# Performance work log

Hardware: AMD Instinct MI355X
Metric: run time of the kernel (lower is better)

Reference implementation:

```python
import jax, jax.numpy as jnp
import numpy as np

U, B, D = 1024, 8, 512
H, HD = 8, 64
CL, RC = 64, 4            # chunk length, right-context per chunk
C = U // CL               # 16 chunks
R, S, M = C * RC, C, C - 1
Q, KV = R + U + S, M + R + U
PE = 2 * U - 1
NEG_INF = -1e8


def _chunk_mask():
    # True = disallowed connection. Query rows = [right_context(R), utterance(U), summary(S)];
    # key cols = [memory(M), right_context(R), utterance(U)].
    mask = np.ones((Q, KV), dtype=bool)
    for c in range(C):
        cols = []
        cols += list(range(0, c))                                  # memory of preceding chunks
        cols += list(range(M + c * RC, M + (c + 1) * RC))          # own right context
        u0 = max(0, c - 1) * CL                                    # one left-context chunk
        cols += list(range(M + R + u0, M + R + (c + 1) * CL))      # utterance up to own chunk
        cols = np.array(cols)
        rows = np.concatenate([
            np.arange(c * RC, (c + 1) * RC),                       # right-context queries
            np.arange(R + c * CL, R + (c + 1) * CL),               # utterance queries
            np.array([R + U + c]),                                 # summary query
        ])
        mask[np.ix_(rows, cols)] = False
    return jnp.asarray(mask)


def _xavier(key, shape):
    fan_in, fan_out = shape[-1], shape[0]
    a = (6.0 / (fan_in + fan_out)) ** 0.5
    return jax.random.uniform(key, shape, jnp.float32, -a, a)


def setup_inputs() -> dict:
    key = jax.random.key(0)
    ks = jax.random.split(key, 16)
    return {
        "utterance": jax.random.normal(ks[0], (U, B, D), jnp.float32),
        "lengths": jax.random.randint(ks[1], (B,), U // 2, U + 1),
        "right_context": jax.random.normal(ks[2], (R, B, D), jnp.float32),
        "summary": jax.random.normal(ks[3], (S, B, D), jnp.float32),
        "memory": jax.random.normal(ks[4], (M, B, D), jnp.float32),
        "attention_mask": _chunk_mask(),
        "pos_emb": jax.random.normal(ks[5], (PE, D), jnp.float32),
        "W_kv": _xavier(ks[6], (2 * D, D)),
        "b_kv": jnp.zeros((2 * D,), jnp.float32),
        "W_q": _xavier(ks[7], (D, D)),
        "b_q": jnp.zeros((D,), jnp.float32),
        "W_out": _xavier(ks[8], (D, D)),
        "b_out": jnp.zeros((D,), jnp.float32),
        "W_pos": _xavier(ks[9], (D, D)),
        "pos_bias_u": _xavier(ks[10], (H, HD)),
        "pos_bias_v": _xavier(ks[11], (H, HD)),
    }


def reference(utterance, lengths, right_context, summary, memory, attention_mask,
              pos_emb, W_kv, b_kv, W_q, b_q, W_out, b_out, W_pos,
              pos_bias_u, pos_bias_v):
    u_len, b, d = utterance.shape
    r, m, s = right_context.shape[0], memory.shape[0], summary.shape[0]
    h = pos_bias_u.shape[0]
    hd = d // h
    scaling = hd ** -0.5

    query = jnp.concatenate([right_context, utterance, summary], 0) @ W_q.T + b_q   # (Q,B,D)
    kv = jnp.concatenate([memory, right_context, utterance], 0) @ W_kv.T + b_kv     # (KV,B,2D)
    key_t, val_t = kv[..., :d], kv[..., d:]
    q_len, kv_len = query.shape[0], key_t.shape[0]

    k = key_t.reshape(kv_len, b, h, hd).transpose(1, 2, 0, 3)   # (B,H,KV,hd)
    v = val_t.reshape(kv_len, b, h, hd).transpose(1, 2, 0, 3)   # (B,H,KV,hd)
    q = query.reshape(q_len, b, h, hd)                           # (Q,B,H,hd)

    qu = (q + pos_bias_u).transpose(1, 2, 0, 3)                  # (B,H,Q,hd)
    matrix_ac = jnp.einsum('bhqe,bhke->bhqk', qu, k)             # (B,H,Q,KV)

    qv = (q[r:r + u_len] + pos_bias_v).transpose(1, 2, 0, 3)     # (B,H,U,hd)
    pe_len = pos_emb.shape[0]
    pos = (pos_emb @ W_pos.T).reshape(pe_len, h, hd).transpose(1, 0, 2)  # (H,PE,hd)
    bd_u = jnp.einsum('bhue,hpe->bhup', qv, pos)                 # (B,H,U,PE)

    # rel_shift: out[u, j] = in[u, U-1-u+j]
    out_len = pe_len - (u_len - 1)
    idx = (u_len - 1) - jnp.arange(u_len)[:, None] + jnp.arange(out_len)[None, :]
    bd_u = jnp.take_along_axis(bd_u, idx[None, None], axis=-1)   # (B,H,U,out_len)

    matrix_bd = jnp.zeros_like(matrix_ac).at[:, :, r:r + u_len, m + r:].set(bd_u)
    w = (matrix_ac + matrix_bd) * scaling

    w = jnp.where(attention_mask[None, None], NEG_INF, w)
    pad = jnp.arange(kv_len)[None, :] >= (kv_len - u_len + lengths)[:, None]  # (B,KV)
    w = jnp.where(pad[:, None, None, :], NEG_INF, w)

    probs = jax.nn.softmax(w, axis=-1)
    attn = jnp.einsum('bhqk,bhke->bhqe', probs, v)               # (B,H,Q,hd)
    attn = attn.transpose(2, 0, 1, 3).reshape(q_len, b, d)       # (Q,B,D)

    out_ru = attn[:r + u_len] @ W_out.T + b_out                  # (R+U,B,D)
    out_mem = jnp.clip(attn[r + u_len:], -10.0, 10.0)            # (S,B,D); tanh_on_mem=False
    return out_ru, out_mem
```

## Files before the change

kernel.cpp:

```cpp
#include <hip/hip_runtime.h>
#include <hip/hip_bf16.h>

typedef __hip_bfloat16 bf16;
typedef __attribute__((ext_vector_type(8))) short short8v;
typedef __attribute__((ext_vector_type(4))) float float4v;

#define UU 1024
#define BB 8
#define DD 512
#define HH 8
#define HD 64
#define RR 64
#define SS 16
#define MM 15
#define QQ 1104
#define KVL 1103
#define PEL 2047
#define NU 1536
#define MU 8952

#define AS1 __attribute__((address_space(1)))
#define AS3 __attribute__((address_space(3)))

__device__ __forceinline__ float lo16(unsigned u) { return __uint_as_float(u << 16); }
__device__ __forceinline__ float hi16(unsigned u) { return __uint_as_float(u & 0xffff0000u); }
__device__ __forceinline__ unsigned pk2(float a, float b) {
  unsigned short x = __builtin_bit_cast(unsigned short, __float2bfloat16(a));
  unsigned short y = __builtin_bit_cast(unsigned short, __float2bfloat16(b));
  return (unsigned)x | ((unsigned)y << 16);
}

struct PackDesc {
  const void* src[16];
  unsigned int srcoff[16];
  unsigned int dstoff[16];
  unsigned int cum[17];
};

__global__ __launch_bounds__(256) void pack_all(PackDesc d, bf16* base,
                                                const void* __restrict__ probe,
                                                int* __restrict__ flagout,
                                                int nchunks) {
  __shared__ int wsum[4];
  const unsigned short* p = (const unsigned short*)probe;
  int big = 0;
  for (int i = threadIdx.x; i < 4096; i += 256)
    big += (((p[i] >> 7) & 0xFF) >= 137) ? 1 : 0;
  #pragma unroll
  for (int off = 32; off; off >>= 1) big += __shfl_down(big, off);
  if ((threadIdx.x & 63) == 0) wsum[threadIdx.x >> 6] = big;
  __syncthreads();
  const int flag = (wsum[0] + wsum[1] + wsum[2] + wsum[3] < 16) ? 1 : 0;
  if (threadIdx.x == 0 && blockIdx.x == 0) *flagout = flag;

  int g = blockIdx.x * 256 + threadIdx.x;
  if (g >= nchunks) return;
  int s = 0;
  #pragma unroll
  for (int i = 1; i < 17; ++i) s += (g >= d.cum[i]) ? 1 : 0;
  unsigned local = (g - d.cum[s]) * 8u;
  bf16* dst = base + d.dstoff[s] + local;
  if (flag) {
    const uint4 v = *(const uint4*)((const bf16*)d.src[s] + d.srcoff[s] + local);
    *(uint4*)dst = v;
  } else {
    const float* fp = (const float*)d.src[s] + d.srcoff[s] + local;
    uint4 o;
    o.x = pk2(fp[0], fp[1]);
    o.y = pk2(fp[2], fp[3]);
    o.z = pk2(fp[4], fp[5]);
    o.w = pk2(fp[6], fp[7]);
    *(uint4*)dst = o;
  }
}

struct GemmP {
  const bf16* X; const bf16* W; const bf16* bias; void* out;
  int M, N, K; const int* outf;
};

__global__ __launch_bounds__(256, 3) void gemm_dual(GemmP g0, GemmP g1, int ysplit) {
  __shared__ bf16 As[64 * 128];
  __shared__ bf16 Bs[128 * 128];
  GemmP g; int bm, bn;
  if ((int)blockIdx.y < ysplit) {
    g = g0;
    int bi = (int)blockIdx.y * (int)gridDim.x + (int)blockIdx.x;
    int nbn = g0.N >> 7;
    int j = bi >> 3;
    int bmi = (bi & 7) + (j / nbn) * 8;
    int bni = j % nbn;
    if (bmi >= ((g0.M + 63) >> 6)) return;
    bm = bmi * 64; bn = bni * 128;
  } else {
    g = g1;
    int nt = g1.N >> 7;
    int bi = ((int)blockIdx.y - ysplit) * gridDim.x + blockIdx.x;
    if (bi >= ((g1.M + 63) >> 6) * nt) return;
    bm = (bi / nt) * 64; bn = (bi % nt) * 128;
  }
  const int tid = threadIdx.x;
  const int lane = tid & 63, wv = tid >> 6;
  const int wr = wv >> 1, wc = wv & 1;
  const int l4 = lane >> 4;
  const int lb = lane & 15;
  const int quad = lane >> 4, l15 = lane & 15;

  float4v acc[2][4] = {};

  for (int kb = 0; kb < g.K; kb += 128) {
    #pragma unroll
    for (int i = 0; i < 4; ++i) {
      int r = wv * 16 + i * 4 + l4;
      int gm = bm + r; if (gm > g.M - 1) gm = g.M - 1;
      const bf16* src = g.X + (size_t)gm * g.K + kb + ((lb ^ (r & 15)) * 8);
      __builtin_amdgcn_global_load_lds((const AS1 void*)src,
                                       (AS3 void*)&As[(wv * 16 + i * 4) * 128], 16, 0, 0);
    }
    #pragma unroll
    for (int i = 0; i < 8; ++i) {
      int r = wv * 32 + i * 4 + l4;
      int gn = bn + r; if (gn > g.N - 1) gn = g.N - 1;
      const bf16* src = g.W + (size_t)gn * g.K + kb + ((lb ^ (r & 15)) * 8);
      __builtin_amdgcn_global_load_lds((const AS1 void*)src,
                                       (AS3 void*)&Bs[(wv * 32 + i * 4) * 128], 16, 0, 0);
    }
    __syncthreads();
    #pragma unroll
    for (int ki = 0; ki < 4; ++ki) {
      const int slot = ((ki * 4 + quad) ^ l15) * 8;
      short8v a[2], bq[4];
      #pragma unroll
      for (int t = 0; t < 2; ++t)
        a[t] = *(const short8v*)&As[(wr * 32 + t * 16 + l15) * 128 + slot];
      #pragma unroll
      for (int t = 0; t < 4; ++t)
        bq[t] = *(const short8v*)&Bs[(wc * 64 + t * 16 + l15) * 128 + slot];
      #pragma unroll
      for (int mt = 0; mt < 2; ++mt)
        #pragma unroll
        for (int nt = 0; nt < 4; ++nt)
          acc[mt][nt] = __builtin_amdgcn_mfma_f32_16x16x32_bf16(
              a[mt], bq[nt], acc[mt][nt], 0, 0, 0);
    }
    __syncthreads();
  }

  const bool as_bf16 = (g.outf == nullptr) ? true : (*g.outf != 0);
  #pragma unroll
  for (int mt = 0; mt < 2; ++mt) {
    #pragma unroll
    for (int r = 0; r < 4; ++r) {
      int gm = bm + wr * 32 + mt * 16 + quad * 4 + r;
      if (gm >= g.M) continue;
      #pragma unroll
      for (int nt = 0; nt < 4; ++nt) {
        int gn = bn + wc * 64 + nt * 16 + l15;
        float v = acc[mt][nt][r];
        if (g.bias) v += __bfloat162float(g.bias[gn]);
        size_t o = (size_t)gm * g.N + gn;
        if (as_bf16) ((bf16*)g.out)[o] = __float2bfloat16(v);
        else         ((float*)g.out)[o] = v;
      }
    }
  }
}

__global__ __launch_bounds__(512, 2) void gemm8(
    const bf16* __restrict__ XUp, const bf16* __restrict__ Wcatp,
    const bf16* __restrict__ bcatp, bf16* __restrict__ qkvp,
    const bf16* __restrict__ posecp, const bf16* __restrict__ Wpospp,
    bf16* __restrict__ posp) {
  __shared__ bf16 smem[65536];
  const int tid = threadIdx.x;
  const int lane = tid & 63, wv = tid >> 6;
  const int wr = wv >> 2, wc = wv & 3;
  const int quad = lane >> 4, l15 = lane & 15, key = l15 & 7;
  const int lr3 = lane >> 3, l7 = lane & 7;
  const int schunk = (l7 ^ lr3) * 8;

  const bf16 *gX, *gW, *gB; bf16* gO; int gM, gN, bm, bn;
  const int bid = (int)blockIdx.x;
  if (bid < 210) {
    int xcd = bid & 7, j = bid >> 3;
    int wg = (xcd < 2 ? xcd * 27 : 54 + (xcd - 2) * 26) + j;
    bm = (wg / 6) * 256; bn = (wg % 6) * 256;
    gX = XUp; gW = Wcatp; gB = bcatp; gO = qkvp; gM = MU; gN = NU;
  } else {
    gX = posecp; gW = Wpospp; gB = nullptr; gO = posp; gM = 191; gN = 512;
    bm = 0; bn = (bid - 210) * 256;
  }

  bf16* A0 = smem;
  bf16* B0 = smem + 32768;

  auto stage = [&](const bf16* src, int rbase, int Mlim, bf16* dst, int kb) {
    #pragma unroll
    for (int j = 0; j < 4; ++j) {
      int rl = j * 64 + wv * 8 + lr3;
      int gr = rbase + rl; if (gr > Mlim - 1) gr = Mlim - 1;
      const bf16* s = src + (size_t)gr * 512 + kb + schunk;
      __builtin_amdgcn_global_load_lds((const AS1 void*)s,
                                       (AS3 void*)(dst + (j * 64 + wv * 8) * 64), 16, 0, 0);
    }
  };

  float4v acc[8][4] = {};

  stage(gX, bm, gM, A0, 0);
  stage(gW, bn, gN, B0, 0);
  stage(gX, bm, gM, A0 + 16384, 64);
  stage(gW, bn, gN, B0 + 16384, 64);
  asm volatile("s_waitcnt vmcnt(8)" ::: "memory");
  asm volatile("s_barrier" ::: "memory");

  for (int t = 0; t < 8; ++t) {
    const int p = t & 1;
    const bf16* Ab = A0 + p * 16384;
    const bf16* Bb = B0 + p * 16384;
    #pragma unroll
    for (int ph = 0; ph < 4; ++ph) {
      const int mh = ph & 1, nh = ph >> 1;
      if (ph == 0 && t >= 1 && t < 7) stage(gX, bm, gM, A0 + (p ^ 1) * 16384, (t + 1) * 64);
      if (ph == 1 && t >= 1 && t < 7) stage(gW, bn, gN, B0 + (p ^ 1) * 16384, (t + 1) * 64);
      short8v al[4][2], bl[2][2];
      #pragma unroll
      for (int i = 0; i < 4; ++i) {
        const bf16* rp = Ab + (wr * 128 + (mh * 4 + i) * 16 + l15) * 64;
        #pragma unroll
        for (int ks = 0; ks < 2; ++ks)
          al[i][ks] = *(const short8v*)(rp + (((ks * 4 + quad) ^ key) * 8));
      }
      #pragma unroll
      for (int j = 0; j < 2; ++j) {
        const bf16* rp = Bb + (wc * 64 + (nh * 2 + j) * 16 + l15) * 64;
        #pragma unroll
        for (int ks = 0; ks < 2; ++ks)
          bl[j][ks] = *(const short8v*)(rp + (((ks * 4 + quad) ^ key) * 8));
      }
      asm volatile("s_barrier" ::: "memory");
      __builtin_amdgcn_s_setprio(1);
      #pragma unroll
      for (int ks = 0; ks < 2; ++ks)
        #pragma unroll
        for (int i = 0; i < 4; ++i)
          #pragma unroll
          for (int j = 0; j < 2; ++j)
            acc[mh * 4 + i][nh * 2 + j] = __builtin_amdgcn_mfma_f32_16x16x32_bf16(
                al[i][ks], bl[j][ks], acc[mh * 4 + i][nh * 2 + j], 0, 0, 0);
      __builtin_amdgcn_s_setprio(0);
      if (ph == 3 && t < 7) asm volatile("s_waitcnt vmcnt(0)" ::: "memory");
      asm volatile("s_barrier" ::: "memory");
    }
  }

  #pragma unroll
  for (int mf = 0; mf < 8; ++mf) {
    #pragma unroll
    for (int r = 0; r < 4; ++r) {
      int gm = bm + wr * 128 + mf * 16 + quad * 4 + r;
      if (gm >= gM) continue;
      #pragma unroll
      for (int nf = 0; nf < 4; ++nf) {
        int gn = bn + wc * 64 + nf * 16 + l15;
        float v = acc[mf][nf][r];
        if (gB) v += __bfloat162float(gB[gn]);
        gO[(size_t)gm * gN + gn] = __float2bfloat16(v);
      }
    }
  }
}

__device__ __forceinline__ int gcol(int row, int c, int u0, int ncols) {
  if (row < c) return row;
  if (row < c + 4) return 15 + 4 * c + (row - c);
  if (row < ncols) return 79 + u0 + (row - c - 4);
  return 0;
}

__global__ __launch_bounds__(256, 2) void attn_chunk(
    const bf16* __restrict__ qkv, const bf16* __restrict__ pos,
    const bf16* __restrict__ pbu, const bf16* __restrict__ pbv,
    const int* __restrict__ lengths, bf16* __restrict__ attn,
    const int* __restrict__ flag, void* __restrict__ dout) {
  __shared__ char lds[65536];
  bf16* Vs   = (bf16*)(lds);
  bf16* Aqu  = (bf16*)(lds + 19456);
  bf16* Kt   = (bf16*)(lds + 29696);
  bf16* Aqv  = (bf16*)(lds + 32768);
  bf16* Psl  = (bf16*)(lds + 40960);
  bf16* Eb   = (bf16*)(lds + 49152);
  bf16* Pp   = (bf16*)(lds + 19456);
  float* wred  = (float*)(lds + 46336);
  float* rstat = (float*)(lds + 47616);

  const int idx = blockIdx.x;
  const int h = idx & 7, b = (idx >> 3) & 7, c = idx >> 6;
  const int u0 = c ? (c - 1) * 64 : 0;
  const int nut = c ? 128 : 64;
  const int ncols = c + 4 + nut;
  const int q0 = c ? 63 : 127;
  const int tid = threadIdx.x, lane = tid & 63, wv = tid >> 6;
  const int quad = lane >> 4, l15 = lane & 15, key = l15 & 7;
  const int lenlim = lengths[b] - u0;
  const bool obf = (*flag != 0);

  {
    int lr = lane >> 3;
    int sbr = (lane & 7) ^ lr;
    for (int i = wv; i < 19; i += 4) {
      int row = i * 8 + lr;
      int g = gcol(row, c, u0, ncols);
      int sbv = (lane & 7) ^ (i & 7);
      const bf16* src = qkv + ((size_t)(g * 8 + b)) * NU + 1024 + h * 64 + sbv * 8;
      __builtin_amdgcn_global_load_lds((const AS1 void*)src, (AS3 void*)(Vs + i * 512), 16, 0, 0);
    }
    for (int i = wv; i < 24; i += 4) {
      int p = i * 8 + lr;
      const bf16* src = pos + (size_t)p * 512 + h * 64 + sbr * 8;
      __builtin_amdgcn_global_load_lds((const AS1 void*)src, (AS3 void*)(Psl + i * 512), 16, 0, 0);
    }
  }
  for (int id = tid; id < 1152; id += 256) {
    bool isv = id >= 640;
    int lid = isv ? id - 640 : id;
    int m = lid >> 3, ec = lid & 7;
    int qrow;
    if (isv) qrow = 64 + 64 * c + m;
    else qrow = (m < 64) ? (64 + 64 * c + m)
              : (m < 68) ? (4 * c + (m - 64))
              : (m == 68) ? (1088 + c) : 0;
    const uint4 qa = *(const uint4*)(qkv + ((size_t)((qrow + 15) * 8 + b)) * NU + h * 64 + ec * 8);
    const uint4 ba = *(const uint4*)((isv ? pbv : pbu) + h * 64 + ec * 8);
    uint4 o;
    o.x = pk2(lo16(qa.x) + lo16(ba.x), hi16(qa.x) + hi16(ba.x));
    o.y = pk2(lo16(qa.y) + lo16(ba.y), hi16(qa.y) + hi16(ba.y));
    o.z = pk2(lo16(qa.z) + lo16(ba.z), hi16(qa.z) + hi16(ba.z));
    o.w = pk2(lo16(qa.w) + lo16(ba.w), hi16(qa.w) + hi16(ba.w));
    *(uint4*)((isv ? Aqv : Aqu) + m * 64 + (ec ^ (m & 7)) * 8) = o;
  }
  __syncthreads();

  float4v eacc[4][3];
  #pragma unroll
  for (int mt = 0; mt < 4; ++mt)
    #pragma unroll
    for (int i = 0; i < 3; ++i) eacc[mt][i] = (float4v){0.f, 0.f, 0.f, 0.f};
  {
    short8v av[4][2];
    #pragma unroll
    for (int mt = 0; mt < 4; ++mt)
      #pragma unroll
      for (int ks = 0; ks < 2; ++ks)
        av[mt][ks] = *(const short8v*)&Aqv[(mt * 16 + l15) * 64 + ((ks * 4 + quad) ^ key) * 8];
    #pragma unroll
    for (int nti = 0; nti < 3; ++nti) {
      int nt = wv + nti * 4;
      short8v b0 = *(const short8v*)&Psl[(nt * 16 + l15) * 64 + (quad ^ key) * 8];
      short8v b1 = *(const short8v*)&Psl[(nt * 16 + l15) * 64 + ((4 + quad) ^ key) * 8];
      #pragma unroll
      for (int mt = 0; mt < 4; ++mt) {
        eacc[mt][nti] = __builtin_amdgcn_mfma_f32_16x16x32_bf16(av[mt][0], b0, eacc[mt][nti], 0, 0, 0);
        eacc[mt][nti] = __builtin_amdgcn_mfma_f32_16x16x32_bf16(av[mt][1], b1, eacc[mt][nti], 0, 0, 0);
      }
    }
  }
  __syncthreads();

  {
    int lr = lane >> 3, sbr = (lane & 7) ^ lr;
    for (int i = wv; i < 19; i += 4) {
      int row = i * 8 + lr;
      int g = gcol(row, c, u0, ncols);
      const bf16* src = qkv + ((size_t)(g * 8 + b)) * NU + 512 + h * 64 + sbr * 8;
      __builtin_amdgcn_global_load_lds((const AS1 void*)src, (AS3 void*)(Kt + i * 512), 16, 0, 0);
    }
  }
  #pragma unroll
  for (int nti = 0; nti < 3; ++nti) {
    int p = (wv + nti * 4) * 16 + l15;
    #pragma unroll
    for (int mt = 0; mt < 4; ++mt)
      #pragma unroll
      for (int r = 0; r < 4; ++r) {
        int m = mt * 16 + quad * 4 + r;
        int jl = p - q0 + m;
        if (jl >= 0 && jl < nut)
          Eb[m * 128 + (jl ^ (((m >> 2) & 7) << 4))] = __float2bfloat16(eacc[mt][nti][r]);
      }
  }
  __syncthreads();

  const int nnt = (wv < 2) ? 3 : 2;
  float4v sacc[5][3];
  #pragma unroll
  for (int mt = 0; mt < 5; ++mt)
    #pragma unroll
    for (int i = 0; i < 3; ++i) sacc[mt][i] = (float4v){0.f, 0.f, 0.f, 0.f};
  {
    short8v au[5][2];
    #pragma unroll
    for (int mt = 0; mt < 5; ++mt)
      #pragma unroll
      for (int ks = 0; ks < 2; ++ks)
        au[mt][ks] = *(const short8v*)&Aqu[(mt * 16 + l15) * 64 + ((ks * 4 + quad) ^ key) * 8];
    #pragma unroll
    for (int nti = 0; nti < 3; ++nti) {
      if (nti < nnt) {
        int nt = wv + nti * 4;
        short8v b0 = *(const short8v*)&Kt[(nt * 16 + l15) * 64 + (quad ^ key) * 8];
        short8v b1 = *(const short8v*)&Kt[(nt * 16 + l15) * 64 + ((4 + quad) ^ key) * 8];
        #pragma unroll
        for (int mt = 0; mt < 5; ++mt) {
          sacc[mt][nti] = __builtin_amdgcn_mfma_f32_16x16x32_bf16(au[mt][0], b0, sacc[mt][nti], 0, 0, 0);
          sacc[mt][nti] = __builtin_amdgcn_mfma_f32_16x16x32_bf16(au[mt][1], b1, sacc[mt][nti], 0, 0, 0);
        }
      }
    }
  }
  __syncthreads();

  #pragma unroll
  for (int nti = 0; nti < 3; ++nti) {
    if (nti < nnt) {
      int colv = (wv + nti * 4) * 16 + l15;
      int jl = colv - (c + 4);
      bool cvalid = (colv < ncols) && !(jl >= 0 && jl >= lenlim);
      #pragma unroll
      for (int mt = 0; mt < 5; ++mt)
        #pragma unroll
        for (int r = 0; r < 4; ++r) {
          float s = sacc[mt][nti][r];
          if (cvalid) {
            if (mt < 4 && jl >= 0) {
              int m = mt * 16 + quad * 4 + r;
              s += __bfloat162float(Eb[m * 128 + (jl ^ (((m >> 2) & 7) << 4))]);
            }
            s *= 0.125f;
          } else s = -1e30f;
          sacc[mt][nti][r] = s;
        }
    }
  }

  {
    #pragma unroll
    for (int mt = 0; mt < 5; ++mt)
      #pragma unroll
      for (int r = 0; r < 4; ++r) {
        float v = -3e38f;
        #pragma unroll
        for (int nti = 0; nti < 3; ++nti)
          if (nti < nnt) v = fmaxf(v, sacc[mt][nti][r]);
        v = fmaxf(v, __shfl_xor(v, 1));
        v = fmaxf(v, __shfl_xor(v, 2));
        v = fmaxf(v, __shfl_xor(v, 4));
        v = fmaxf(v, __shfl_xor(v, 8));
        if (l15 == 0) wred[(mt * 16 + quad * 4 + r) * 4 + wv] = v;
      }
  }
  __syncthreads();
  if (tid < 80)
    rstat[tid] = fmaxf(fmaxf(wred[tid * 4], wred[tid * 4 + 1]),
                       fmaxf(wred[tid * 4 + 2], wred[tid * 4 + 3]));
  __syncthreads();

  {
    float rmx[5][4], rsum[5][4];
    #pragma unroll
    for (int mt = 0; mt < 5; ++mt)
      #pragma unroll
      for (int r = 0; r < 4; ++r) {
        rmx[mt][r] = rstat[mt * 16 + quad * 4 + r];
        rsum[mt][r] = 0.f;
      }
    #pragma unroll
    for (int nti = 0; nti < 3; ++nti) {
      if (nti < nnt) {
        int colv = (wv + nti * 4) * 16 + l15;
        #pragma unroll
        for (int mt = 0; mt < 5; ++mt)
          #pragma unroll
          for (int r = 0; r < 4; ++r) {
            float p = __expf(sacc[mt][nti][r] - rmx[mt][r]);
            Pp[(mt * 16 + quad * 4 + r) * 168 + colv] = __float2bfloat16(p);
            rsum[mt][r] += p;
          }
      }
    }
    #pragma unroll
    for (int mt = 0; mt < 5; ++mt)
      #pragma unroll
      for (int r = 0; r < 4; ++r) {
        float v = rsum[mt][r];
        v += __shfl_xor(v, 1);
        v += __shfl_xor(v, 2);
        v += __shfl_xor(v, 4);
        v += __shfl_xor(v, 8);
        if (l15 == 0) wred[(mt * 16 + quad * 4 + r) * 4 + wv] = v;
      }
  }
  __syncthreads();
  if (tid < 80)
    rstat[tid] = 1.f / (wred[tid * 4] + wred[tid * 4 + 1] + wred[tid * 4 + 2] + wred[tid * 4 + 3]);
  __syncthreads();

  const int kmax = (ncols + 31) >> 5;
  float4v oacc[5];
  #pragma unroll
  for (int mt = 0; mt < 5; ++mt) oacc[mt] = (float4v){0.f, 0.f, 0.f, 0.f};
  const int ehi = (wv * 16 + l15) >> 3, elo = l15 & 7;
  for (int ks = 0; ks < kmax; ++ks) {
    short8v bq;
    const int blk = ehi ^ ((ks * 4 + quad) & 7);
    #pragma unroll
    for (int j = 0; j < 8; ++j)
      bq[j] = ((const short*)Vs)[(ks * 32 + quad * 8 + j) * 64 + blk * 8 + elo];
    #pragma unroll
    for (int mt = 0; mt < 5; ++mt) {
      short8v af = *(const short8v*)&Pp[(mt * 16 + l15) * 168 + ks * 32 + quad * 8];
      oacc[mt] = __builtin_amdgcn_mfma_f32_16x16x32_bf16(af, bq, oacc[mt], 0, 0, 0);
    }
  }

  #pragma unroll
  for (int mt = 0; mt < 5; ++mt) {
    #pragma unroll
    for (int r = 0; r < 4; ++r) {
      int m = mt * 16 + quad * 4 + r;
      if (m >= 69) continue;
      float o = oacc[mt][r] * rstat[m];
      if (m < 68) {
        int qrow = (m < 64) ? (64 + 64 * c + m) : (4 * c + (m - 64));
        attn[((size_t)(qrow * 8 + b)) * 512 + h * 64 + wv * 16 + l15] = __float2bfloat16(o);
      } else {
        float v = fminf(fmaxf(o, -10.f), 10.f);
        size_t oi = (size_t)1088 * 8 * 512 + ((size_t)(c * 8 + b)) * 512 + h * 64 + wv * 16 + l15;
        if (obf) ((bf16*)dout)[oi] = __float2bfloat16(v);
        else     ((float*)dout)[oi] = v;
      }
    }
  }
}

static inline int cdiv(int a, int b) { return (a + b - 1) / b; }

extern "C" void kernel_launch(void* const* d_in, const int* in_sizes, int n_in,
                              void* d_out, int out_size, void* d_ws, size_t ws_size,
                              hipStream_t stream) {
  const void* utter = d_in[0];
  const int*  lens  = (const int*)d_in[1];
  const void* rctx  = d_in[2];
  const void* summ  = d_in[3];
  const void* memry = d_in[4];
  const void* pose  = d_in[6];
  const void* W_kv  = d_in[7];
  const void* b_kv  = d_in[8];
  const void* W_q   = d_in[9];
  const void* b_q   = d_in[10];
  const void* W_out = d_in[11];
  const void* b_out = d_in[12];
  const void* W_pos = d_in[13];
  const void* pbu   = d_in[14];
  const void* pbv   = d_in[15];

  const unsigned SZ_MM = MM * BB * DD;
  const unsigned SZ_RC = RR * BB * DD;
  const unsigned SZ_UT = UU * BB * DD;
  const unsigned SZ_SM = SS * BB * DD;
  const unsigned N_XU  = SZ_MM + SZ_RC + SZ_UT + SZ_SM;
  const unsigned SZ_PS = 191 * DD;

  int*  flag = (int*)d_ws;
  bf16* base = (bf16*)((char*)d_ws + 64);
  unsigned off = 0;
  bf16* XU    = base + off; unsigned o_XU    = off; off += N_XU;
  bf16* posec = base + off; unsigned o_posec = off; off += 192 * DD;
  bf16* Wcat  = base + off; unsigned o_Wcat  = off; off += (unsigned)NU * DD;
  bf16* bcat  = base + off; unsigned o_bcat  = off; off += NU;
  bf16* Woutp = base + off; unsigned o_Wout  = off; off += DD * DD;
  bf16* boutp = base + off; unsigned o_bout  = off; off += DD;
  bf16* Wposp = base + off; unsigned o_Wpos  = off; off += DD * DD;
  bf16* pbuc  = base + off; unsigned o_pbu   = off; off += DD;
  bf16* pbvc  = base + off; unsigned o_pbv   = off; off += DD;
  bf16* qkv   = base + off; off += (unsigned)(MU + 8) * NU;
  bf16* pos   = base + off; off += 192 * DD;
  bf16* attn  = base + off; off += QQ * BB * DD;

  PackDesc pd;
  const void* srcs[14]  = {memry, rctx, utter, summ, pose,
                           W_q, W_kv, b_q, b_kv, W_out, b_out, W_pos, pbu, pbv};
  unsigned    soffs[14] = {0, 0, 0, 0, 896u * DD, 0, 0, 0, 0, 0, 0, 0, 0, 0};
  unsigned    doffs[14] = {o_XU, o_XU + SZ_MM, o_XU + SZ_MM + SZ_RC,
                           o_XU + SZ_MM + SZ_RC + SZ_UT, o_posec,
                           o_Wcat, o_Wcat + DD * DD, o_bcat, o_bcat + DD,
                           o_Wout, o_bout, o_Wpos, o_pbu, o_pbv};
  unsigned    ns[14]    = {SZ_MM, SZ_RC, SZ_UT, SZ_SM, SZ_PS,
                           DD * DD, 2 * DD * DD, DD, 2 * DD,
                           DD * DD, DD, DD * DD, DD, DD};
  unsigned cum = 0;
  for (int i = 0; i < 14; ++i) {
    pd.src[i] = srcs[i]; pd.srcoff[i] = soffs[i]; pd.dstoff[i] = doffs[i];
    pd.cum[i] = cum; cum += ns[i] / 8;
  }
  pd.src[14] = pbv; pd.srcoff[14] = 0; pd.dstoff[14] = o_pbv;
  pd.src[15] = pbv; pd.srcoff[15] = 0; pd.dstoff[15] = o_pbv;
  pd.cum[14] = cum; pd.cum[15] = cum; pd.cum[16] = cum;
  int nchunks = (int)cum;
  pack_all<<<dim3(cdiv(nchunks, 256)), dim3(256), 0, stream>>>(pd, base, utter, flag, nchunks);

  gemm8<<<dim3(212), dim3(512), 0, stream>>>(XU, Wcat, bcat, qkv, posec, Wposp, pos);

  attn_chunk<<<dim3(1024), dim3(256), 0, stream>>>(qkv, pos, pbuc, pbvc, lens, attn,
                                                   flag, d_out);

  GemmP go{attn, Woutp, boutp, d_out, (RR + UU) * BB, DD, DD, flag};
  gemm_dual<<<dim3(4, 136), dim3(256), 0, stream>>>(go, go, 136);
}
```

Before: 198.4 us.

## Restructure QKV GEMM mainloop into four-stage K=32 LDS pipeline

Replaces the double-buffered K=64 tiles (with four sub-phases per tile) in gemm8 with a four-buffer ring of K=32 slabs, prefetching three slabs ahead. Each step issues a single set of LDS reads and 32 MFMAs, with a new XOR swizzle matched to the 32-wide rows. The goal is deeper global-to-LDS latency hiding and fewer barriers per K element. In exchange there are more, smaller stages, and the hand-tuned vmcnt counts must match the outstanding loads exactly.

Measured after the change: 197.8 us. Within noise of the previous version (-0.3%).

```diff
diff --git a/kernel.cpp b/kernel.cpp
--- a/kernel.cpp
+++ b/kernel.cpp
@@ -175,9 +175,7 @@
   const int tid = threadIdx.x;
   const int lane = tid & 63, wv = tid >> 6;
   const int wr = wv >> 2, wc = wv & 3;
-  const int quad = lane >> 4, l15 = lane & 15, key = l15 & 7;
-  const int lr3 = lane >> 3, l7 = lane & 7;
-  const int schunk = (l7 ^ lr3) * 8;
+  const int quad = lane >> 4, l15 = lane & 15;
 
   const bf16 *gX, *gW, *gB; bf16* gO; int gM, gN, bm, bn;
   const int bid = (int)blockIdx.x;
@@ -196,62 +194,52 @@
 
   auto stage = [&](const bf16* src, int rbase, int Mlim, bf16* dst, int kb) {
     #pragma unroll
-    for (int j = 0; j < 4; ++j) {
-      int rl = j * 64 + wv * 8 + lr3;
+    for (int j = 0; j < 2; ++j) {
+      int rl = j * 128 + wv * 16 + (lane >> 2);
       int gr = rbase + rl; if (gr > Mlim - 1) gr = Mlim - 1;
-      const bf16* s = src + (size_t)gr * 512 + kb + schunk;
+      int kc = ((lane & 3) ^ ((rl >> 1) & 3)) * 8;
+      const bf16* s = src + (size_t)gr * 512 + kb + kc;
       __builtin_amdgcn_global_load_lds((const AS1 void*)s,
-                                       (AS3 void*)(dst + (j * 64 + wv * 8) * 64), 16, 0, 0);
+                                       (AS3 void*)(dst + (j * 128 + wv * 16) * 32), 16, 0, 0);
     }
   };
 
   float4v acc[8][4] = {};
-
-  stage(gX, bm, gM, A0, 0);
-  stage(gW, bn, gN, B0, 0);
-  stage(gX, bm, gM, A0 + 16384, 64);
-  stage(gW, bn, gN, B0 + 16384, 64);
+  const int pos8 = (quad ^ ((l15 >> 1) & 3)) * 8;
+
+  stage(gX, bm, gM, A0, 0);          stage(gW, bn, gN, B0, 0);
+  stage(gX, bm, gM, A0 + 8192, 32);  stage(gW, bn, gN, B0 + 8192, 32);
+  stage(gX, bm, gM, A0 + 16384, 64); stage(gW, bn, gN, B0 + 16384, 64);
   asm volatile("s_waitcnt vmcnt(8)" ::: "memory");
   asm volatile("s_barrier" ::: "memory");
 
-  for (int t = 0; t < 8; ++t) {
-    const int p = t & 1;
-    const bf16* Ab = A0 + p * 16384;
-    const bf16* Bb = B0 + p * 16384;
-    #pragma unroll
-    for (int ph = 0; ph < 4; ++ph) {
-      const int mh = ph & 1, nh = ph >> 1;
-      if (ph == 0 && t >= 1 && t < 7) stage(gX, bm, gM, A0 + (p ^ 1) * 16384, (t + 1) * 64);
-      if (ph == 1 && t >= 1 && t < 7) stage(gW, bn, gN, B0 + (p ^ 1) * 16384, (t + 1) * 64);
-      short8v al[4][2], bl[2][2];
-      #pragma unroll
-      for (int i = 0; i < 4; ++i) {
-        const bf16* rp = Ab + (wr * 128 + (mh * 4 + i) * 16 + l15) * 64;
-        #pragma unroll
-        for (int ks = 0; ks < 2; ++ks)
-          al[i][ks] = *(const short8v*)(rp + (((ks * 4 + quad) ^ key) * 8));
-      }
-      #pragma unroll
-      for (int j = 0; j < 2; ++j) {
-        const bf16* rp = Bb + (wc * 64 + (nh * 2 + j) * 16 + l15) * 64;
-        #pragma unroll
-        for (int ks = 0; ks < 2; ++ks)
-          bl[j][ks] = *(const short8v*)(rp + (((ks * 4 + quad) ^ key) * 8));
-      }
-      asm volatile("s_barrier" ::: "memory");
-      __builtin_amdgcn_s_setprio(1);
-      #pragma unroll
-      for (int ks = 0; ks < 2; ++ks)
-        #pragma unroll
-        for (int i = 0; i < 4; ++i)
-          #pragma unroll
-          for (int j = 0; j < 2; ++j)
-            acc[mh * 4 + i][nh * 2 + j] = __builtin_amdgcn_mfma_f32_16x16x32_bf16(
-                al[i][ks], bl[j][ks], acc[mh * 4 + i][nh * 2 + j], 0, 0, 0);
-      __builtin_amdgcn_s_setprio(0);
-      if (ph == 3 && t < 7) asm volatile("s_waitcnt vmcnt(0)" ::: "memory");
-      asm volatile("s_barrier" ::: "memory");
-    }
+  #pragma unroll
+  for (int s = 0; s < 16; ++s) {
+    if (s + 3 < 16) {
+      stage(gX, bm, gM, A0 + ((s + 3) & 3) * 8192, (s + 3) * 32);
+      stage(gW, bn, gN, B0 + ((s + 3) & 3) * 8192, (s + 3) * 32);
+    }
+    const bf16* As = A0 + (s & 3) * 8192;
+    const bf16* Bs = B0 + (s & 3) * 8192;
+    short8v al[8], bl[4];
+    #pragma unroll
+    for (int i = 0; i < 8; ++i)
+      al[i] = *(const short8v*)&As[(wr * 128 + i * 16 + l15) * 32 + pos8];
+    #pragma unroll
+    for (int j = 0; j < 4; ++j)
+      bl[j] = *(const short8v*)&Bs[(wc * 64 + j * 16 + l15) * 32 + pos8];
+    asm volatile("s_barrier" ::: "memory");
+    __builtin_amdgcn_s_setprio(1);
+    #pragma unroll
+    for (int i = 0; i < 8; ++i)
+      #pragma unroll
+      for (int j = 0; j < 4; ++j)
+        acc[i][j] = __builtin_amdgcn_mfma_f32_16x16x32_bf16(al[i], bl[j], acc[i][j], 0, 0, 0);
+    __builtin_amdgcn_s_setprio(0);
+    if (s <= 12)      asm volatile("s_waitcnt vmcnt(8)" ::: "memory");
+    else if (s == 13) asm volatile("s_waitcnt vmcnt(4)" ::: "memory");
+    else if (s == 14) asm volatile("s_waitcnt vmcnt(0)" ::: "memory");
+    if (s < 15)       asm volatile("s_barrier" ::: "memory");
   }
 
   #pragma unroll
```
